# Kernel optimization log

Measured on AMD Instinct MI355X. Metric: run time of the kernel, lower is better.

## Reference

```python
import jax, jax.numpy as jnp
import numpy as np

B, N, DIM = 32, 1024, 512
HEADS, HEAD_DIM = 8, 64
MLP_HIDDEN = 2048
MAX_DIST = 7
TABLE_SIZE = (2 * MAX_DIST + 1) ** 2  # 225


def setup_inputs() -> dict:
    key = jax.random.key(0)
    ks = jax.random.split(key, 8)
    return {
        "x": jax.random.normal(ks[0], (B, N, DIM), jnp.float32),
        "qkv_w": jax.random.normal(ks[1], (3 * DIM, DIM), jnp.float32) * 0.02,
        "proj_w": jax.random.normal(ks[2], (DIM, DIM), jnp.float32) * 0.02,
        "proj_b": jnp.zeros((DIM,), jnp.float32),
        "mlp_w1": jax.random.normal(ks[3], (MLP_HIDDEN, DIM), jnp.float32) * 0.02,
        "mlp_b1": jnp.zeros((MLP_HIDDEN,), jnp.float32),
        "mlp_w2": jax.random.normal(ks[4], (DIM, MLP_HIDDEN), jnp.float32) * 0.02,
        "mlp_b2": jnp.zeros((DIM,), jnp.float32),
        "norm1_g": jnp.ones((DIM,), jnp.float32),
        "norm1_b": jnp.zeros((DIM,), jnp.float32),
        "norm2_g": jnp.ones((DIM,), jnp.float32),
        "norm2_b": jnp.zeros((DIM,), jnp.float32),
        "bias_table": jax.random.normal(ks[5], (TABLE_SIZE, HEADS), jnp.float32) * 0.02,
        "height": 32,
        "width": 32,
    }


def _rel_pos_index(height, width):
    # exact replication of RelativePositionBias index math (numpy, trace-time)
    coords = np.stack(np.meshgrid(np.arange(height), np.arange(width), indexing="ij"))  # [2,H,W]
    flat = coords.reshape(2, -1)                         # [2,N]
    rel = flat[:, :, None] - flat[:, None, :]            # [2,N,N]
    rel = rel.transpose(1, 2, 0).copy()                  # [N,N,2]
    rel[:, :, 0] += height - 1
    rel[:, :, 1] += width - 1
    rel[:, :, 0] *= 2 * width - 1
    idx = np.clip(rel.sum(-1), 0, TABLE_SIZE - 1)
    return jnp.asarray(idx, jnp.int32)                   # [N,N]


def _layernorm(x, g, b, eps=1e-5):
    mu = x.mean(-1, keepdims=True)
    var = ((x - mu) ** 2).mean(-1, keepdims=True)
    return (x - mu) * jax.lax.rsqrt(var + eps) * g + b


def reference(x, qkv_w, proj_w, proj_b, mlp_w1, mlp_b1, mlp_w2, mlp_b2,
              norm1_g, norm1_b, norm2_g, norm2_b, bias_table, height, width):
    scale = HEAD_DIM ** -0.5
    idx = _rel_pos_index(height, width)
    bias = bias_table[idx]                               # [N,N,heads]
    bias = jnp.transpose(bias, (2, 0, 1))                # [heads,N,N]

    shortcut = x
    h = _layernorm(x, norm1_g, norm1_b)
    qkv = h @ qkv_w.T                                    # [B,N,3*DIM]
    qkv = qkv.reshape(x.shape[0], x.shape[1], 3, HEADS, HEAD_DIM)
    qkv = jnp.transpose(qkv, (2, 0, 3, 1, 4))            # [3,B,h,N,d]
    q, k, v = qkv[0], qkv[1], qkv[2]
    attn = jnp.einsum("bhnd,bhmd->bhnm", q, k) * scale
    attn = attn + bias[None]
    attn = jax.nn.softmax(attn, axis=-1)
    o = jnp.einsum("bhnm,bhmd->bhnd", attn, v)           # [B,h,N,d]
    o = jnp.transpose(o, (0, 2, 1, 3)).reshape(x.shape)  # [B,N,DIM]
    o = o @ proj_w.T + proj_b
    x = shortcut + o

    shortcut = x
    h = _layernorm(x, norm2_g, norm2_b)
    h = jax.nn.gelu(h @ mlp_w1.T + mlp_b1, approximate=False)
    h = h @ mlp_w2.T + mlp_b2
    return shortcut + h
```

## Files before the change

kernel.cpp:

```cpp
#include <hip/hip_runtime.h>

typedef short bf16x8 __attribute__((ext_vector_type(8)));
typedef float f32x4 __attribute__((ext_vector_type(4)));
typedef unsigned short us8 __attribute__((ext_vector_type(8)));
typedef unsigned short us2 __attribute__((ext_vector_type(2)));

__device__ __forceinline__ float bf2f(unsigned short u) {
    union { unsigned i; float f; } v; v.i = ((unsigned)u) << 16; return v.f;
}
__device__ __forceinline__ unsigned short f2bf(float f) {
    union { float f; unsigned i; } v; v.f = f;
    unsigned r = v.i + 0x7fffu + ((v.i >> 16) & 1u);
    return (unsigned short)(r >> 16);
}
__device__ __forceinline__ float ldflex(const void* p, int isf32, long i) {
    return isf32 ? ((const float*)p)[i] : bf2f(((const unsigned short*)p)[i]);
}
__device__ __forceinline__ float gelu_exact(float v) {
    return 0.5f * v * (1.0f + erff(v * 0.70710678118654752f));
}
__device__ __forceinline__ us8 pack8u(const float* s) {
    us8 r;
    #pragma unroll
    for (int i = 0; i < 8; ++i) r[i] = f2bf(s[i]);
    return r;
}

__device__ __forceinline__ void gld16(const void* g, void* l) {
    typedef __attribute__((address_space(1))) void GV;
    typedef __attribute__((address_space(3))) void LV;
    __builtin_amdgcn_global_load_lds((GV*)g, (LV*)l, 16, 0, 0);
}

struct SniffArgs { const void* p[13]; int n[13]; };

__global__ __launch_bounds__(64) void sniff_all(SniffArgs a, int* __restrict__ flags)
{
    const unsigned short* buf = (const unsigned short*)a.p[blockIdx.x];
    const int n_elems = a.n[blockIdx.x];
    __shared__ int cnt[3];
    if (threadIdx.x < 3) cnt[threadIdx.x] = 0;
    __syncthreads();
    int K = n_elems / 2; if (K > 1024) K = 1024; if (K < 1) K = 1;
    int ins = 0, ne = 0, no = 0;
    for (int i = threadIdx.x; i < K; i += 64) {
        const unsigned lo = buf[2 * i], hi = buf[2 * i + 1];
        const unsigned e = (lo >> 7) & 0xFF;
        ins += (lo != 0 && (e < 90 || e > 160)) ? 1 : 0;
        ne  += (lo != 0);
        no  += (hi != 0);
    }
    atomicAdd(&cnt[0], ins); atomicAdd(&cnt[1], ne); atomicAdd(&cnt[2], no);
    __syncthreads();
    if (threadIdx.x == 0)
        flags[blockIdx.x] = (cnt[0] * 10 > K) || (cnt[1] * 10 < K && cnt[2] * 2 > K);
}

struct CvtArgs { const void* src[7]; void* dst[7]; int fidx[7]; int n[7]; int tobf[7]; };

__global__ __launch_bounds__(256) void convert_params(CvtArgs a, const int* __restrict__ flags)
{
    const int t = blockIdx.y;
    const int i0 = (blockIdx.x * 256 + threadIdx.x) * 8;
    if (i0 >= a.n[t]) return;
    const int f = flags[a.fidx[t]];
    float v[8];
    if (f) {
        const float* s = (const float*)a.src[t] + i0;
        *(f32x4*)&v[0] = *(const f32x4*)s;
        *(f32x4*)&v[4] = *(const f32x4*)(s + 4);
    } else {
        us8 u = *(const us8*)((const unsigned short*)a.src[t] + i0);
        #pragma unroll
        for (int i = 0; i < 8; ++i) v[i] = bf2f(u[i]);
    }
    if (a.tobf[t]) {
        *(us8*)((unsigned short*)a.dst[t] + i0) = pack8u(v);
    } else {
        float* d = (float*)a.dst[t] + i0;
        *(f32x4*)d       = *(f32x4*)&v[0];
        *(f32x4*)(d + 4) = *(f32x4*)&v[4];
    }
}

__global__ __launch_bounds__(256) void gemm_bf16(
    const unsigned short* __restrict__ A, const unsigned short* __restrict__ W,
    void* __restrict__ C, int Nout, int K,
    const float* __restrict__ bias,
    const void* resid, const int* rflag, long resid_row0,
    int act, int out_bf16)
{
    __shared__ unsigned short As[128 * 32];
    __shared__ unsigned short Bs[128 * 32];
    const int tid  = threadIdx.x;
    const int lane = tid & 63, wv = tid >> 6;
    const int wrow = wv >> 1, wcol = wv & 1;
    const int fm = lane & 15, quad = lane >> 4;

    const int gx = gridDim.x;
    const int nwg = gx * gridDim.y;
    int lin = blockIdx.y * gx + blockIdx.x;
    lin = (lin & 7) * (nwg >> 3) + (lin >> 3);
    const int bm = (lin / gx) * 128, bn = (lin % gx) * 128;

    const int sr = tid >> 2;
    const int sb = (tid & 3) * 16;
    const char* Ab = (const char*)A;
    const char* Wb = (const char*)W;
    char* AsB = (char*)As;
    char* BsB = (char*)Bs;
    const long a0 = ((long)(bm + sr) * K) * 2 + sb;
    const long a1 = ((long)(bm + 64 + sr) * K) * 2 + sb;
    const long b0 = ((long)(bn + sr) * K) * 2 + sb;
    const long b1 = ((long)(bn + 64 + sr) * K) * 2 + sb;
    const int ld = tid * 16;

    f32x4 acc[4][4] = {};

    const int Kb = K * 2;
    for (int k0b = 0; k0b < Kb; k0b += 64) {
        __syncthreads();
        gld16(Ab + a0 + k0b, AsB + ld);
        gld16(Ab + a1 + k0b, AsB + 4096 + ld);
        gld16(Wb + b0 + k0b, BsB + ld);
        gld16(Wb + b1 + k0b, BsB + 4096 + ld);
        __syncthreads();

        bf16x8 af[4], bw[4];
        #pragma unroll
        for (int t = 0; t < 4; ++t) {
            af[t] = *(const bf16x8*)&As[(wrow * 64 + t * 16 + fm) * 32 + quad * 8];
            bw[t] = *(const bf16x8*)&Bs[(wcol * 64 + t * 16 + fm) * 32 + quad * 8];
        }
        #pragma unroll
        for (int i = 0; i < 4; ++i)
            #pragma unroll
            for (int j = 0; j < 4; ++j)
                acc[i][j] = __builtin_amdgcn_mfma_f32_16x16x32_bf16(
                                af[i], bw[j], acc[i][j], 0, 0, 0);
    }

    const int crow0 = bm + wrow * 64, ccol0 = bn + wcol * 64;
    if (out_bf16) {
        unsigned short* Cb = (unsigned short*)C;
        #pragma unroll
        for (int j = 0; j < 4; ++j) {
            const int col = ccol0 + j * 16 + fm;
            const float bv = bias ? bias[col] : 0.0f;
            #pragma unroll
            for (int i = 0; i < 4; ++i)
                #pragma unroll
                for (int r = 0; r < 4; ++r) {
                    const int row = crow0 + i * 16 + quad * 4 + r;
                    float v = acc[i][j][r] + bv;
                    if (act) v = gelu_exact(v);
                    Cb[(long)row * Nout + col] = f2bf(v);
                }
        }
    } else {
        float* Cf = (float*)C;
        const int rfl = resid ? (rflag ? *rflag : 1) : 1;
        #pragma unroll
        for (int j = 0; j < 4; ++j) {
            const int col = ccol0 + j * 16 + fm;
            const float bv = bias ? bias[col] : 0.0f;
            #pragma unroll
            for (int i = 0; i < 4; ++i)
                #pragma unroll
                for (int r = 0; r < 4; ++r) {
                    const int row = crow0 + i * 16 + quad * 4 + r;
                    float v = acc[i][j][r] + bv;
                    if (act)   v = gelu_exact(v);
                    if (resid) v += ldflex(resid, rfl, (resid_row0 + row) * (long)Nout + col);
                    Cf[(long)row * Nout + col] = v;
                }
        }
    }
}

__global__ __launch_bounds__(256) void layernorm_512(
    const void* __restrict__ x, const int* __restrict__ xflag, long row0,
    const void* __restrict__ g, const int* __restrict__ gflag,
    const void* __restrict__ b, const int* __restrict__ bflag,
    unsigned short* __restrict__ o)
{
    const int row = blockIdx.x;
    const int tid = threadIdx.x;
    const int xf = xflag ? *xflag : 1;
    const long base = (row0 + row) * 512 + tid * 2;
    const float vx = ldflex(x, xf, base);
    const float vy = ldflex(x, xf, base + 1);
    float s  = vx + vy;
    float s2 = vx * vx + vy * vy;
    #pragma unroll
    for (int off = 32; off > 0; off >>= 1) {
        s  += __shfl_down(s, off);
        s2 += __shfl_down(s2, off);
    }
    __shared__ float ss[4], ss2[4];
    if ((tid & 63) == 0) { ss[tid >> 6] = s; ss2[tid >> 6] = s2; }
    __syncthreads();
    const float ts   = ss[0] + ss[1] + ss[2] + ss[3];
    const float ts2  = ss2[0] + ss2[1] + ss2[2] + ss2[3];
    const float mean = ts * (1.0f / 512.0f);
    const float var  = ts2 * (1.0f / 512.0f) - mean * mean;
    const float rstd = rsqrtf(var + 1e-5f);
    const int gf = *gflag, bff = *bflag;
    us2 r;
    r[0] = f2bf((vx - mean) * rstd * ldflex(g, gf, tid * 2)     + ldflex(b, bff, tid * 2));
    r[1] = f2bf((vy - mean) * rstd * ldflex(g, gf, tid * 2 + 1) + ldflex(b, bff, tid * 2 + 1));
    *(us2*)(o + (long)row * 512 + tid * 2) = r;
}

__global__ __launch_bounds__(256, 3) void attn_mfma(
    const unsigned short* __restrict__ qkv,
    const void* __restrict__ table, const int* __restrict__ tflag,
    unsigned short* __restrict__ o)
{
    __shared__ unsigned short Ks[64 * 72];
    __shared__ unsigned short Vt[64 * 72];
    __shared__ unsigned short Pl[4][16 * 72];
    __shared__ float Tb[1800];

    const int tid  = threadIdx.x;
    const int lane = tid & 63, wv = tid >> 6;
    const int fm = lane & 15, quad = lane >> 4;
    const int q0 = blockIdx.x * 64;
    const int h  = blockIdx.y;
    const int b  = blockIdx.z;

    {
        const int tf = *tflag;
        for (int i = tid; i < 1800; i += 256) Tb[i] = ldflex(table, tf, i);
    }

    bf16x8 qa[2];
    {
        const unsigned short* qb = &qkv[(long)((b * 1024 + q0 + wv * 16 + fm) * 3) * 512
                                        + h * 64 + quad * 8];
        qa[0] = *(const bf16x8*)qb;
        qa[1] = *(const bf16x8*)(qb + 32);
    }

    f32x4 acc[4] = {};
    float mrow[4] = {-1e30f, -1e30f, -1e30f, -1e30f};
    float lrow[4] = {};

    const int key_s = tid >> 2;
    const int dc    = (tid & 3) * 16;

    for (int kt = 0; kt < 16; ++kt) {
        const int k0 = kt * 64;
        __syncthreads();
        {
            const unsigned short* kp =
                &qkv[((long)((b * 1024 + k0 + key_s) * 3) + 1) * 512 + h * 64 + dc];
            *(us8*)&Ks[key_s * 72 + dc]     = *(const us8*)kp;
            *(us8*)&Ks[key_s * 72 + dc + 8] = *(const us8*)(kp + 8);
            const unsigned short* vp =
                &qkv[((long)((b * 1024 + k0 + key_s) * 3) + 2) * 512 + h * 64 + dc];
            us8 v0 = *(const us8*)vp, v1 = *(const us8*)(vp + 8);
            #pragma unroll
            for (int i = 0; i < 8; ++i) {
                Vt[(dc + i) * 72 + key_s]     = v0[i];
                Vt[(dc + 8 + i) * 72 + key_s] = v1[i];
            }
        }
        __syncthreads();

        f32x4 sv[4];
        __builtin_amdgcn_s_setprio(1);
        #pragma unroll
        for (int c = 0; c < 4; ++c) {
            f32x4 z = {};
            z = __builtin_amdgcn_mfma_f32_16x16x32_bf16(
                    qa[0], *(const bf16x8*)&Ks[(c * 16 + fm) * 72 + quad * 8], z, 0, 0, 0);
            z = __builtin_amdgcn_mfma_f32_16x16x32_bf16(
                    qa[1], *(const bf16x8*)&Ks[(c * 16 + fm) * 72 + 32 + quad * 8], z, 0, 0, 0);
            sv[c] = z;
        }
        __builtin_amdgcn_s_setprio(0);

        #pragma unroll
        for (int c = 0; c < 4; ++c) {
            const int kj = k0 + c * 16 + fm;
            const int ky = kj >> 5, kx = kj & 31;
            #pragma unroll
            for (int r = 0; r < 4; ++r) {
                const int qi = q0 + wv * 16 + quad * 4 + r;
                const int dy = (qi >> 5) - ky;
                const int dx = (qi & 31) - kx;
                int idx = (dy + 31) * 63 + (dx + 31);
                idx = idx > 224 ? 224 : idx;
                sv[c][r] = sv[c][r] * 0.125f + Tb[idx * 8 + h];
            }
        }

        float alpha[4];
        #pragma unroll
        for (int r = 0; r < 4; ++r) {
            float mr = fmaxf(fmaxf(sv[0][r], sv[1][r]), fmaxf(sv[2][r], sv[3][r]));
            #pragma unroll
            for (int off = 1; off < 16; off <<= 1) mr = fmaxf(mr, __shfl_xor(mr, off));
            const float mnew = fmaxf(mrow[r], mr);
            alpha[r] = __expf(mrow[r] - mnew);
            mrow[r] = mnew;
            float ps = 0.0f;
            #pragma unroll
            for (int c = 0; c < 4; ++c) {
                const float p = __expf(sv[c][r] - mnew);
                sv[c][r] = p;
                ps += p;
            }
            #pragma unroll
            for (int off = 1; off < 16; off <<= 1) ps += __shfl_xor(ps, off);
            lrow[r] = lrow[r] * alpha[r] + ps;
        }

        unsigned short* Pw = Pl[wv];
        #pragma unroll
        for (int c = 0; c < 4; ++c)
            #pragma unroll
            for (int r = 0; r < 4; ++r)
                Pw[(quad * 4 + r) * 72 + c * 16 + fm] = f2bf(sv[c][r]);

        const bf16x8 ap0 = *(const bf16x8*)&Pw[fm * 72 + quad * 8];
        const bf16x8 ap1 = *(const bf16x8*)&Pw[fm * 72 + 32 + quad * 8];
        __builtin_amdgcn_s_setprio(1);
        #pragma unroll
        for (int c = 0; c < 4; ++c) {
            #pragma unroll
            for (int r = 0; r < 4; ++r) acc[c][r] *= alpha[r];
            acc[c] = __builtin_amdgcn_mfma_f32_16x16x32_bf16(
                        ap0, *(const bf16x8*)&Vt[(c * 16 + fm) * 72 + quad * 8], acc[c], 0, 0, 0);
            acc[c] = __builtin_amdgcn_mfma_f32_16x16x32_bf16(
                        ap1, *(const bf16x8*)&Vt[(c * 16 + fm) * 72 + 32 + quad * 8], acc[c], 0, 0, 0);
        }
        __builtin_amdgcn_s_setprio(0);
    }

    float rinv[4];
    #pragma unroll
    for (int r = 0; r < 4; ++r) rinv[r] = 1.0f / lrow[r];
    #pragma unroll
    for (int c = 0; c < 4; ++c)
        #pragma unroll
        for (int r = 0; r < 4; ++r)
            o[(long)(b * 1024 + q0 + wv * 16 + quad * 4 + r) * 512 + h * 64 + c * 16 + fm]
                = f2bf(acc[c][r] * rinv[r]);
}

extern "C" void kernel_launch(void* const* d_in, const int* in_sizes, int n_in,
                              void* d_out, int out_size, void* d_ws, size_t ws_size,
                              hipStream_t stream)
{
    (void)n_in; (void)out_size;
    float* out = (float*)d_out;

    constexpr int B = 32, N = 1024;

    int* flags = (int*)d_ws;
    {
        SniffArgs sa;
        for (int t = 0; t < 13; ++t) { sa.p[t] = d_in[t]; sa.n[t] = in_sizes[t]; }
        sniff_all<<<13, 64, 0, stream>>>(sa, flags);
    }

    unsigned short* Wq = (unsigned short*)((char*)d_ws + 256);
    unsigned short* Wp = Wq + 786432;
    unsigned short* W1 = Wp + 262144;
    unsigned short* W2 = W1 + 1048576;
    float* Bp = (float*)(W2 + 1048576);
    float* B1 = Bp + 512;
    float* B2 = B1 + 2048;
    char* scr = (char*)(B2 + 512);
    scr = (char*)(((size_t)scr + 255) & ~(size_t)255);

    {
        CvtArgs ca;
        ca.src[0] = d_in[1]; ca.dst[0] = Wq; ca.fidx[0] = 1; ca.n[0] = 786432;  ca.tobf[0] = 1;
        ca.src[1] = d_in[2]; ca.dst[1] = Wp; ca.fidx[1] = 2; ca.n[1] = 262144;  ca.tobf[1] = 1;
        ca.src[2] = d_in[4]; ca.dst[2] = W1; ca.fidx[2] = 4; ca.n[2] = 1048576; ca.tobf[2] = 1;
        ca.src[3] = d_in[6]; ca.dst[3] = W2; ca.fidx[3] = 6; ca.n[3] = 1048576; ca.tobf[3] = 1;
        ca.src[4] = d_in[3]; ca.dst[4] = Bp; ca.fidx[4] = 3; ca.n[4] = 512;     ca.tobf[4] = 0;
        ca.src[5] = d_in[5]; ca.dst[5] = B1; ca.fidx[5] = 5; ca.n[5] = 2048;    ca.tobf[5] = 0;
        ca.src[6] = d_in[7]; ca.dst[6] = B2; ca.fidx[6] = 7; ca.n[6] = 512;     ca.tobf[6] = 0;
        convert_params<<<dim3(512, 7), 256, 0, stream>>>(ca, flags);
    }

    const size_t fixed = (size_t)(scr - (char*)d_ws);
    const size_t per_batch = (size_t)N * 3072 * 2;
    int bpc = (int)((ws_size - fixed) / per_batch);
    if (bpc < 1) bpc = 1;
    if (bpc > B) bpc = B;

    unsigned short* Ln = (unsigned short*)scr;
    unsigned short* Hd = Ln + (size_t)bpc * N * 512;
    unsigned short* Ao = Hd + (size_t)bpc * N * 2048;

    for (int b0 = 0; b0 < B; b0 += bpc) {
        const int nb   = (B - b0) < bpc ? (B - b0) : bpc;
        const int rows = nb * N;
        const long r0  = (long)b0 * N;

        layernorm_512<<<rows, 256, 0, stream>>>(
            d_in[0], flags + 0, r0, d_in[8], flags + 8, d_in[9], flags + 9, Ln);
        gemm_bf16<<<dim3(12, rows / 128), 256, 0, stream>>>(
            Ln, Wq, Hd, 1536, 512, nullptr, nullptr, nullptr, 0, 0, 1);
        attn_mfma<<<dim3(16, 8, nb), 256, 0, stream>>>(
            Hd, d_in[12], flags + 12, Ao);
        gemm_bf16<<<dim3(4, rows / 128), 256, 0, stream>>>(
            Ao, Wp, out + r0 * 512, 512, 512,
            Bp, d_in[0], flags + 0, r0, 0, 0);
    }

    for (int b0 = 0; b0 < B; b0 += bpc) {
        const int nb   = (B - b0) < bpc ? (B - b0) : bpc;
        const int rows = nb * N;
        const long r0  = (long)b0 * N;

        layernorm_512<<<rows, 256, 0, stream>>>(
            out + r0 * 512, nullptr, 0, d_in[10], flags + 10, d_in[11], flags + 11, Ln);
        gemm_bf16<<<dim3(16, rows / 128), 256, 0, stream>>>(
            Ln, W1, Hd, 2048, 512, B1, nullptr, nullptr, 0, 1, 1);
        gemm_bf16<<<dim3(4, rows / 128), 256, 0, stream>>>(
            Hd, W2, out + r0 * 512, 512, 2048,
            B2, out + r0 * 512, nullptr, 0, 0, 0);
    }
}
```

Before: 976.8 us.

## Direct-to-LDS K loads, per-head bias table, grid swizzle, higher occupancy

The attention kernel now loads K tiles with direct global-to-LDS 16-byte loads (gld16) into an MFMA-fragment-ordered layout, so the register staging and padded copy go away. It stages only the current head's 225 bias entries instead of the full 1800-entry table. The bias index is derived from a precomputed per-row base, and the 1D block index is remapped so that consecutive blocks spread across heads and batches. Launch bounds rise from 3 to 5 blocks per CU, which trades register budget for occupancy and risks spills.

```diff
diff --git a/kernel.cpp b/kernel.cpp
--- a/kernel.cpp
+++ b/kernel.cpp
@@ -212,26 +212,30 @@
     *(us2*)(o + (long)row * 512 + tid * 2) = r;
 }
 
-__global__ __launch_bounds__(256, 3) void attn_mfma(
+__global__ __launch_bounds__(256, 5) void attn_mfma(
     const unsigned short* __restrict__ qkv,
     const void* __restrict__ table, const int* __restrict__ tflag,
     unsigned short* __restrict__ o)
 {
-    __shared__ unsigned short Ks[64 * 72];
+    __shared__ unsigned short Ks[512 * 8];
     __shared__ unsigned short Vt[64 * 72];
     __shared__ unsigned short Pl[4][16 * 72];
-    __shared__ float Tb[1800];
+    __shared__ float Tbh[225];
 
     const int tid  = threadIdx.x;
     const int lane = tid & 63, wv = tid >> 6;
     const int fm = lane & 15, quad = lane >> 4;
-    const int q0 = blockIdx.x * 64;
-    const int h  = blockIdx.y;
-    const int b  = blockIdx.z;
+
+    const int hw    = blockIdx.x + gridDim.x * (blockIdx.y + gridDim.y * blockIdx.z);
+    const int total = gridDim.x * gridDim.y * gridDim.z;
+    const int lin   = (hw & 7) * (total >> 3) + (hw >> 3);
+    const int q0 = (lin & 15) * 64;
+    const int h  = (lin >> 4) & 7;
+    const int b  = lin >> 7;
 
     {
         const int tf = *tflag;
-        for (int i = tid; i < 1800; i += 256) Tb[i] = ldflex(table, tf, i);
+        if (tid < 225) Tbh[tid] = ldflex(table, tf, tid * 8 + h);
     }
 
     bf16x8 qa[2];
@@ -242,30 +246,43 @@
         qa[1] = *(const bf16x8*)(qb + 32);
     }
 
+    int base_r[4];
+    #pragma unroll
+    for (int r = 0; r < 4; ++r) {
+        const int qi = q0 + wv * 16 + quad * 4 + r;
+        base_r[r] = 63 * (qi >> 5) + (qi & 31) + 1984;
+    }
+
+    const int kc_fm   = tid & 15;
+    const int kc_quad = (tid >> 4) & 3;
+    const int kc_ch   = (tid >> 6) & 1;
+    const int kc_c0   = (tid >> 7) & 1;
+    const char* qkvB  = (const char*)qkv;
+    long ksrc = (((long)(b * 1024 + kc_c0 * 16 + kc_fm) * 3 + 1) * 512
+                 + h * 64 + kc_ch * 32 + kc_quad * 8) * 2;
+
+    const int key_v = tid & 63;
+    const int dv    = (tid >> 6) * 16;
+    long vsrc = (((long)(b * 1024 + key_v) * 3 + 2) * 512 + h * 64 + dv) * 2;
+
+    char* KsB = (char*)Ks;
+
     f32x4 acc[4] = {};
     float mrow[4] = {-1e30f, -1e30f, -1e30f, -1e30f};
     float lrow[4] = {};
 
-    const int key_s = tid >> 2;
-    const int dc    = (tid & 3) * 16;
-
     for (int kt = 0; kt < 16; ++kt) {
         const int k0 = kt * 64;
         __syncthreads();
-        {
-            const unsigned short* kp =
-                &qkv[((long)((b * 1024 + k0 + key_s) * 3) + 1) * 512 + h * 64 + dc];
-            *(us8*)&Ks[key_s * 72 + dc]     = *(const us8*)kp;
-            *(us8*)&Ks[key_s * 72 + dc + 8] = *(const us8*)(kp + 8);
-            const unsigned short* vp =
-                &qkv[((long)((b * 1024 + k0 + key_s) * 3) + 2) * 512 + h * 64 + dc];
-            us8 v0 = *(const us8*)vp, v1 = *(const us8*)(vp + 8);
-            #pragma unroll
-            for (int i = 0; i < 8; ++i) {
-                Vt[(dc + i) * 72 + key_s]     = v0[i];
-                Vt[(dc + 8 + i) * 72 + key_s] = v1[i];
-            }
-        }
+        us8 v0 = *(const us8*)(qkvB + vsrc);
+        us8 v1 = *(const us8*)(qkvB + vsrc + 16);
+        gld16(qkvB + ksrc,         KsB + tid * 16);
+        gld16(qkvB + ksrc + 98304, KsB + 4096 + tid * 16);
+        ksrc += 196608; vsrc += 196608;
+        #pragma unroll
+        for (int i = 0; i < 8; ++i) Vt[(dv + i) * 72 + key_v] = v0[i];
+        #pragma unroll
+        for (int i = 0; i < 8; ++i) Vt[(dv + 8 + i) * 72 + key_v] = v1[i];
         __syncthreads();
 
         f32x4 sv[4];
@@ -274,9 +291,11 @@
         for (int c = 0; c < 4; ++c) {
             f32x4 z = {};
             z = __builtin_amdgcn_mfma_f32_16x16x32_bf16(
-                    qa[0], *(const bf16x8*)&Ks[(c * 16 + fm) * 72 + quad * 8], z, 0, 0, 0);
+                    qa[0], *(const bf16x8*)&Ks[(((c * 2 + 0) * 4 + quad) * 16 + fm) * 8],
+                    z, 0, 0, 0);
             z = __builtin_amdgcn_mfma_f32_16x16x32_bf16(
-                    qa[1], *(const bf16x8*)&Ks[(c * 16 + fm) * 72 + 32 + quad * 8], z, 0, 0, 0);
+                    qa[1], *(const bf16x8*)&Ks[(((c * 2 + 1) * 4 + quad) * 16 + fm) * 8],
+                    z, 0, 0, 0);
             sv[c] = z;
         }
         __builtin_amdgcn_s_setprio(0);
@@ -284,15 +303,12 @@
         #pragma unroll
         for (int c = 0; c < 4; ++c) {
             const int kj = k0 + c * 16 + fm;
-            const int ky = kj >> 5, kx = kj & 31;
+            const int sub = 63 * (kj >> 5) + (kj & 31);
             #pragma unroll
             for (int r = 0; r < 4; ++r) {
-                const int qi = q0 + wv * 16 + quad * 4 + r;
-                const int dy = (qi >> 5) - ky;
-                const int dx = (qi & 31) - kx;
-                int idx = (dy + 31) * 63 + (dx + 31);
+                int idx = base_r[r] - sub;
                 idx = idx > 224 ? 224 : idx;
-                sv[c][r] = sv[c][r] * 0.125f + Tb[idx * 8 + h];
+                sv[c][r] = fmaf(sv[c][r], 0.125f, Tbh[idx]);
             }
         }
 
```

Measured after the change: 938.9 us. 1.04x faster.
